# Kernel optimization log

Measured on AMD Instinct MI355X. Metric: run time of the kernel, lower is better.

## Reference

```python
import jax, jax.numpy as jnp
import numpy as np

N_NODES = 40000
N_EDGES = 640000
NFEAT = 128
NHID = 64  # gc1: NFEAT -> 2*NHID, gc2: 2*NHID -> NHID


def setup_inputs() -> dict:
    key = jax.random.key(0)
    ks = jax.random.split(key, 8)
    x = jax.random.normal(ks[0], (N_NODES, NFEAT), dtype=jnp.float32)
    edge_src = jax.random.randint(ks[1], (N_EDGES,), 0, N_NODES, dtype=jnp.int32)
    edge_dst = jax.random.randint(ks[2], (N_EDGES,), 0, N_NODES, dtype=jnp.int32)
    # normalized adjacency weights (e.g. D^-1/2 A D^-1/2 values), positive
    edge_weight = jax.random.uniform(ks[3], (N_EDGES,), dtype=jnp.float32)
    # Glorot-style init as in Kipf GraphConvolution (uniform +- 1/sqrt(fan_out))
    W1 = jax.random.uniform(ks[4], (NFEAT, 2 * NHID), dtype=jnp.float32,
                            minval=-1.0 / np.sqrt(2 * NHID), maxval=1.0 / np.sqrt(2 * NHID))
    b1 = jnp.zeros((2 * NHID,), dtype=jnp.float32)
    W2 = jax.random.uniform(ks[5], (2 * NHID, NHID), dtype=jnp.float32,
                            minval=-1.0 / np.sqrt(NHID), maxval=1.0 / np.sqrt(NHID))
    b2 = jnp.zeros((NHID,), dtype=jnp.float32)
    return {"x": x, "edge_src": edge_src, "edge_dst": edge_dst,
            "edge_weight": edge_weight, "W1": W1, "b1": b1, "W2": W2, "b2": b2}


def _gcn_layer(h, edge_src, edge_dst, edge_weight, W, b, n_nodes):
    # support = h @ W  (dense GEMM), then out = spmm(adj, support) + b
    support = h @ W                                   # [N, Dout]
    msgs = edge_weight[:, None] * support[edge_src]   # [E, Dout] gather
    agg = jax.ops.segment_sum(msgs, edge_dst, num_segments=n_nodes)  # scatter-add
    return agg + b


def reference(x, edge_src, edge_dst, edge_weight, W1, b1, W2, b2):
    n = x.shape[0]
    # gc1 -> relu -> dropout(eval: identity) -> gc2
    h = jax.nn.relu(_gcn_layer(x, edge_src, edge_dst, edge_weight, W1, b1, n))
    out = _gcn_layer(h, edge_src, edge_dst, edge_weight, W2, b2, n)
    return out
```

## Files before the change

kernel.cpp:

```cpp
#include <hip/hip_runtime.h>

#define N_NODES 40000
#define N_EDGES 640000
#define NFEAT   128
#define H1      128
#define H2      64

#define NBUCK   625
#define BCAP    2048
#define EPB     4096

#define OFF_SUP1   0UL
#define OFF_H      10240000UL
#define OFF_SUP2   20480000UL
#define OFF_BUCK   25600000UL
#define OFF_GCUR   35840000UL
#define OFF_W1T    35842560UL
#define OFF_W2T    35875328UL

typedef unsigned int uint;
typedef unsigned short ushort;
typedef __attribute__((ext_vector_type(8))) short bf16x8;
typedef __attribute__((ext_vector_type(4))) float f32x4;
typedef __attribute__((ext_vector_type(2))) float f32x2;

__device__ __forceinline__ float bl(uint u) { union { uint i; float f; } c; c.i = u << 16; return c.f; }
__device__ __forceinline__ float bh(uint u) { union { uint i; float f; } c; c.i = u & 0xFFFF0000u; return c.f; }
__device__ __forceinline__ ushort f2b(float f) {
    union { float f; uint i; } c; c.f = f;
    uint u = c.i + 0x7FFFu + ((c.i >> 16) & 1u);
    return (ushort)(u >> 16);
}

__global__ void init_k(uint* __restrict__ gcur,
                       const float* __restrict__ W1, const float* __restrict__ W2,
                       ushort* __restrict__ W1T, ushort* __restrict__ W2T) {
    const int i = blockIdx.x * 256 + threadIdx.x;
    if (i < NBUCK + 1) gcur[i] = 0;
    if (i < 128 * 128) {
        const int c = i >> 7, k = i & 127;
        W1T[i] = f2b(W1[k * 128 + c]);
    }
    if (i < 64 * 128) {
        const int c = i >> 7, k = i & 127;
        W2T[i] = f2b(W2[k * 64 + c]);
    }
}

__global__ __launch_bounds__(1024) void bin_k(const int* __restrict__ edst,
                                              const int* __restrict__ esrc,
                                              const float* __restrict__ ew,
                                              uint* __restrict__ gcur,
                                              uint2* __restrict__ buckets) {
    __shared__ uint2 stage[EPB];
    __shared__ uint cntL[NBUCK + 1];
    __shared__ uint offL[NBUCK + 1];
    __shared__ uint gbase[NBUCK + 1];
    __shared__ int wsum[16];
    const int t = threadIdx.x;
    const int lane = t & 63, wv = t >> 6;

    if (t < NBUCK + 1) cntL[t] = 0;
    __syncthreads();

    uint d_[4], rec_[4], rk_[4]; int b_[4];
#pragma unroll
    for (int k = 0; k < 4; ++k) {
        const int i = blockIdx.x * EPB + k * 1024 + t;
        uint d = 40000, rec = 0;
        if (i < N_EDGES) {
            d = (uint)edst[i];
            rec = ((uint)esrc[i] << 16) | (uint)f2b(ew[i]);
        }
        d_[k] = d; rec_[k] = rec; b_[k] = d >> 6;
        rk_[k] = atomicAdd(&cntL[b_[k]], 1u);
    }
    __syncthreads();

    {
        const int v = (t < NBUCK + 1) ? (int)cntL[t] : 0;
        int incl = v;
#pragma unroll
        for (int d = 1; d < 64; d <<= 1) {
            int o = __shfl_up(incl, d);
            if (lane >= d) incl += o;
        }
        if (lane == 63) wsum[wv] = incl;
        __syncthreads();
        if (t < 16) {
            int s = wsum[t];
#pragma unroll
            for (int d = 1; d < 16; d <<= 1) {
                int o = __shfl_up(s, d);
                if (t >= d) s += o;
            }
            wsum[t] = s;
        }
        __syncthreads();
        if (t < NBUCK + 1) {
            offL[t] = (uint)((wv ? wsum[wv - 1] : 0) + incl - v);
            gbase[t] = atomicAdd(&gcur[t], (uint)v);
        }
    }
    __syncthreads();

#pragma unroll
    for (int k = 0; k < 4; ++k) {
        uint2 s; s.x = d_[k]; s.y = rec_[k];
        stage[offL[b_[k]] + rk_[k]] = s;
    }
    __syncthreads();

#pragma unroll
    for (int k = 0; k < 4; ++k) {
        const int p = k * 1024 + t;
        const uint2 s = stage[p];
        const uint b = s.x >> 6;
        if (b < NBUCK) {
            const uint pos = gbase[b] + ((uint)p - offL[b]);
            if (pos < BCAP) buckets[(size_t)b * BCAP + pos] = s;
        }
    }
}

__global__ __launch_bounds__(256) void gemm1_k(const float* __restrict__ x,
                                               const ushort* __restrict__ WT,
                                               ushort* __restrict__ out) {
    const int lane = threadIdx.x & 63;
    const int m0 = blockIdx.x * 64 + (threadIdx.x >> 6) * 16;
    const int r = lane & 15, kg = lane >> 4;

    bf16x8 a[4];
    const float* xp = x + (size_t)(m0 + r) * 128 + kg * 8;
#pragma unroll
    for (int kt = 0; kt < 4; ++kt) {
        float xf[8];
        *(float4*)(xf)     = *(const float4*)(xp + kt * 32);
        *(float4*)(xf + 4) = *(const float4*)(xp + kt * 32 + 4);
        bf16x8 v;
#pragma unroll
        for (int i = 0; i < 8; ++i) v[i] = (short)f2b(xf[i]);
        a[kt] = v;
    }

#pragma unroll
    for (int nt = 0; nt < 8; ++nt) {
        const ushort* wp = WT + (size_t)(nt * 16 + r) * 128 + kg * 8;
        f32x4 acc = {0.f, 0.f, 0.f, 0.f};
#pragma unroll
        for (int kt = 0; kt < 4; ++kt) {
            const bf16x8 bfr = *(const bf16x8*)(wp + kt * 32);
            acc = __builtin_amdgcn_mfma_f32_16x16x32_bf16(a[kt], bfr, acc, 0, 0, 0);
        }
#pragma unroll
        for (int q = 0; q < 4; ++q)
            out[(size_t)(m0 + kg * 4 + q) * 128 + nt * 16 + r] = f2b(acc[q]);
    }
}

__global__ __launch_bounds__(256) void gemm2_k(const ushort* __restrict__ h,
                                               const ushort* __restrict__ WT,
                                               ushort* __restrict__ out) {
    const int lane = threadIdx.x & 63;
    const int m0 = blockIdx.x * 64 + (threadIdx.x >> 6) * 16;
    const int r = lane & 15, kg = lane >> 4;

    bf16x8 a[4];
    const ushort* hp = h + (size_t)(m0 + r) * 128 + kg * 8;
#pragma unroll
    for (int kt = 0; kt < 4; ++kt) a[kt] = *(const bf16x8*)(hp + kt * 32);

#pragma unroll
    for (int nt = 0; nt < 4; ++nt) {
        const ushort* wp = WT + (size_t)(nt * 16 + r) * 128 + kg * 8;
        f32x4 acc = {0.f, 0.f, 0.f, 0.f};
#pragma unroll
        for (int kt = 0; kt < 4; ++kt) {
            const bf16x8 bfr = *(const bf16x8*)(wp + kt * 32);
            acc = __builtin_amdgcn_mfma_f32_16x16x32_bf16(a[kt], bfr, acc, 0, 0, 0);
        }
#pragma unroll
        for (int q = 0; q < 4; ++q)
            out[(size_t)(m0 + kg * 4 + q) * 64 + nt * 16 + r] = f2b(acc[q]);
    }
}

__global__ __launch_bounds__(1024) void spmm1_k(const ushort* __restrict__ sup,
                                                const uint* __restrict__ gcur,
                                                const uint2* __restrict__ buckets,
                                                const float* __restrict__ b1,
                                                ushort* __restrict__ h) {
    __shared__ uint srt[BCAP];
    __shared__ uint cntL[64];
    __shared__ uint offL[64];
    const int t = threadIdx.x;
    const int bkt = blockIdx.x;
    if (t < 64) cntL[t] = 0;
    __syncthreads();

    const int cnt = min((int)gcur[bkt], BCAP);
    const uint2* bp = buckets + (size_t)bkt * BCAP;

    int n0 = -1, n1 = -1; uint rec0 = 0, rec1 = 0, rk0 = 0, rk1 = 0;
    if (t < cnt)        { const uint2 r = bp[t];        n0 = r.x & 63; rec0 = r.y; rk0 = atomicAdd(&cntL[n0], 1u); }
    if (t + 1024 < cnt) { const uint2 r = bp[t + 1024]; n1 = r.x & 63; rec1 = r.y; rk1 = atomicAdd(&cntL[n1], 1u); }
    __syncthreads();

    if (t < 64) {
        const int v = (int)cntL[t];
        int incl = v;
#pragma unroll
        for (int d = 1; d < 64; d <<= 1) {
            int o = __shfl_up(incl, d);
            if (t >= d) incl += o;
        }
        offL[t] = (uint)(incl - v);
    }
    __syncthreads();

    if (n0 >= 0) srt[offL[n0] + rk0] = rec0;
    if (n1 >= 0) srt[offL[n1] + rk1] = rec1;
    __syncthreads();

    const int lane = t & 63, wv = t >> 6;
    const uint* sup32 = (const uint*)sup;
    uint* h32 = (uint*)h;
    const float2 bb = ((const float2*)b1)[lane];
#pragma unroll
    for (int j = 0; j < 4; ++j) {
        const int n = wv * 4 + j;
        const int e0 = (int)offL[n], c = (int)cntL[n];
        float a0 = 0.f, a1 = 0.f, a2 = 0.f, a3 = 0.f;
        int e = 0;
        for (; e + 8 <= c; e += 8) {
            uint r[8], v[8];
#pragma unroll
            for (int k = 0; k < 8; ++k) r[k] = srt[e0 + e + k];
#pragma unroll
            for (int k = 0; k < 8; ++k) v[k] = sup32[((size_t)(r[k] >> 16) << 6) + lane];
#pragma unroll
            for (int k = 0; k < 8; k += 2) {
                const float w0 = bl(r[k]), w1 = bl(r[k + 1]);
                a0 = fmaf(w0, bl(v[k]), a0);     a1 = fmaf(w0, bh(v[k]), a1);
                a2 = fmaf(w1, bl(v[k + 1]), a2); a3 = fmaf(w1, bh(v[k + 1]), a3);
            }
        }
        for (; e + 4 <= c; e += 4) {
            uint r[4], v[4];
#pragma unroll
            for (int k = 0; k < 4; ++k) r[k] = srt[e0 + e + k];
#pragma unroll
            for (int k = 0; k < 4; ++k) v[k] = sup32[((size_t)(r[k] >> 16) << 6) + lane];
#pragma unroll
            for (int k = 0; k < 4; k += 2) {
                const float w0 = bl(r[k]), w1 = bl(r[k + 1]);
                a0 = fmaf(w0, bl(v[k]), a0);     a1 = fmaf(w0, bh(v[k]), a1);
                a2 = fmaf(w1, bl(v[k + 1]), a2); a3 = fmaf(w1, bh(v[k + 1]), a3);
            }
        }
        for (; e < c; ++e) {
            const uint r0 = srt[e0 + e];
            const uint v0 = sup32[((size_t)(r0 >> 16) << 6) + lane];
            a0 = fmaf(bl(r0), bl(v0), a0); a1 = fmaf(bl(r0), bh(v0), a1);
        }
        const float f0 = fmaxf((a0 + a2) + bb.x, 0.f);
        const float f1 = fmaxf((a1 + a3) + bb.y, 0.f);
        h32[(size_t)(bkt * 64 + n) * 64 + lane] = (uint)f2b(f0) | ((uint)f2b(f1) << 16);
    }
}

__global__ __launch_bounds__(1024) void spmm2_k(const ushort* __restrict__ sup,
                                                const uint* __restrict__ gcur,
                                                const uint2* __restrict__ buckets,
                                                const float* __restrict__ b2,
                                                float* __restrict__ out) {
    __shared__ uint srt[BCAP];
    __shared__ uint cntL[64];
    __shared__ uint offL[64];
    const int t = threadIdx.x;
    const int bkt = blockIdx.x;
    if (t < 64) cntL[t] = 0;
    __syncthreads();

    const int cnt = min((int)gcur[bkt], BCAP);
    const uint2* bp = buckets + (size_t)bkt * BCAP;

    int n0 = -1, n1 = -1; uint rec0 = 0, rec1 = 0, rk0 = 0, rk1 = 0;
    if (t < cnt)        { const uint2 r = bp[t];        n0 = r.x & 63; rec0 = r.y; rk0 = atomicAdd(&cntL[n0], 1u); }
    if (t + 1024 < cnt) { const uint2 r = bp[t + 1024]; n1 = r.x & 63; rec1 = r.y; rk1 = atomicAdd(&cntL[n1], 1u); }
    __syncthreads();

    if (t < 64) {
        const int v = (int)cntL[t];
        int incl = v;
#pragma unroll
        for (int d = 1; d < 64; d <<= 1) {
            int o = __shfl_up(incl, d);
            if (t >= d) incl += o;
        }
        offL[t] = (uint)(incl - v);
    }
    __syncthreads();

    if (n0 >= 0) srt[offL[n0] + rk0] = rec0;
    if (n1 >= 0) srt[offL[n1] + rk1] = rec1;
    __syncthreads();

    const int lane = t & 63, wv = t >> 6;
    const int hh = lane >> 5, l32 = lane & 31;
    const uint* sup32 = (const uint*)sup;
    const float2 bb = ((const float2*)b2)[l32];
#pragma unroll
    for (int j = 0; j < 4; ++j) {
        const int n = wv * 4 + j;
        const int e0 = (int)offL[n], c = (int)cntL[n];
        float d0 = 0.f, d1 = 0.f, d2 = 0.f, d3 = 0.f;
        int e = 0;
        for (; e + 8 <= c; e += 8) {
            const uint r0 = srt[e0 + e + hh],     r1 = srt[e0 + e + 2 + hh];
            const uint r2 = srt[e0 + e + 4 + hh], r3 = srt[e0 + e + 6 + hh];
            const uint v0 = sup32[((size_t)(r0 >> 16) << 5) + l32];
            const uint v1 = sup32[((size_t)(r1 >> 16) << 5) + l32];
            const uint v2 = sup32[((size_t)(r2 >> 16) << 5) + l32];
            const uint v3 = sup32[((size_t)(r3 >> 16) << 5) + l32];
            d0 = fmaf(bl(r0), bl(v0), d0); d1 = fmaf(bl(r0), bh(v0), d1);
            d2 = fmaf(bl(r1), bl(v1), d2); d3 = fmaf(bl(r1), bh(v1), d3);
            d0 = fmaf(bl(r2), bl(v2), d0); d1 = fmaf(bl(r2), bh(v2), d1);
            d2 = fmaf(bl(r3), bl(v3), d2); d3 = fmaf(bl(r3), bh(v3), d3);
        }
        for (; e + 2 <= c; e += 2) {
            const uint r0 = srt[e0 + e + hh];
            const uint v0 = sup32[((size_t)(r0 >> 16) << 5) + l32];
            d0 = fmaf(bl(r0), bl(v0), d0); d1 = fmaf(bl(r0), bh(v0), d1);
        }
        if (e < c && hh == 0) {
            const uint r0 = srt[e0 + e];
            const uint v0 = sup32[((size_t)(r0 >> 16) << 5) + l32];
            d0 = fmaf(bl(r0), bl(v0), d0); d1 = fmaf(bl(r0), bh(v0), d1);
        }
        float g0 = d0 + d2, g1 = d1 + d3;
        g0 += __shfl_xor(g0, 32); g1 += __shfl_xor(g1, 32);
        if (hh == 0) {
            f32x2 res = {g0 + bb.x, g1 + bb.y};
            __builtin_nontemporal_store(res, (f32x2*)out + (size_t)(bkt * 64 + n) * 32 + l32);
        }
    }
}

extern "C" void kernel_launch(void* const* d_in, const int* in_sizes, int n_in,
                              void* d_out, int out_size, void* d_ws, size_t ws_size,
                              hipStream_t stream) {
    const float* x    = (const float*)d_in[0];
    const int*   esrc = (const int*)d_in[1];
    const int*   edst = (const int*)d_in[2];
    const float* ew   = (const float*)d_in[3];
    const float* W1   = (const float*)d_in[4];
    const float* b1   = (const float*)d_in[5];
    const float* W2   = (const float*)d_in[6];
    const float* b2   = (const float*)d_in[7];
    float* out = (float*)d_out;

    char* ws = (char*)d_ws;
    ushort* sup1    = (ushort*)(ws + OFF_SUP1);
    ushort* h       = (ushort*)(ws + OFF_H);
    ushort* sup2    = (ushort*)(ws + OFF_SUP2);
    uint2*  buckets = (uint2*)(ws + OFF_BUCK);
    uint*   gcur    = (uint*)(ws + OFF_GCUR);
    ushort* W1T     = (ushort*)(ws + OFF_W1T);
    ushort* W2T     = (ushort*)(ws + OFF_W2T);

    init_k<<<64, 256, 0, stream>>>(gcur, W1, W2, W1T, W2T);
    bin_k<<<157, 1024, 0, stream>>>(edst, esrc, ew, gcur, buckets);

    gemm1_k<<<625, 256, 0, stream>>>(x, W1T, sup1);
    spmm1_k<<<NBUCK, 1024, 0, stream>>>(sup1, gcur, buckets, b1, h);

    gemm2_k<<<625, 256, 0, stream>>>(h, W2T, sup2);
    spmm2_k<<<NBUCK, 1024, 0, stream>>>(sup2, gcur, buckets, b2, out);
}
```

Measured before the change: 88.53 us.

## Fuse GEMM1 into binning launch and GEMM2 into first SpMM epilogue

```diff
diff --git a/kernel.cpp b/kernel.cpp
--- a/kernel.cpp
+++ b/kernel.cpp
@@ -9,14 +9,15 @@
 #define NBUCK   625
 #define BCAP    2048
 #define EPB     4096
+#define NBINB   157
+#define HPAD    68
 
 #define OFF_SUP1   0UL
-#define OFF_H      10240000UL
-#define OFF_SUP2   20480000UL
-#define OFF_BUCK   25600000UL
-#define OFF_GCUR   35840000UL
-#define OFF_W1T    35842560UL
-#define OFF_W2T    35875328UL
+#define OFF_SUP2   10240000UL
+#define OFF_BUCK   15360000UL
+#define OFF_GCUR   25600000UL
+#define OFF_W1T    25602560UL
+#define OFF_W2T    25635328UL
 
 typedef unsigned int uint;
 typedef unsigned short ushort;
@@ -47,11 +48,14 @@
     }
 }
 
-__global__ __launch_bounds__(1024) void bin_k(const int* __restrict__ edst,
-                                              const int* __restrict__ esrc,
-                                              const float* __restrict__ ew,
-                                              uint* __restrict__ gcur,
-                                              uint2* __restrict__ buckets) {
+__global__ __launch_bounds__(1024) void bingemm_k(const int* __restrict__ edst,
+                                                  const int* __restrict__ esrc,
+                                                  const float* __restrict__ ew,
+                                                  uint* __restrict__ gcur,
+                                                  uint2* __restrict__ buckets,
+                                                  const float* __restrict__ x,
+                                                  const ushort* __restrict__ W1T,
+                                                  ushort* __restrict__ sup1) {
     __shared__ uint2 stage[EPB];
     __shared__ uint cntL[NBUCK + 1];
     __shared__ uint offL[NBUCK + 1];
@@ -60,6 +64,40 @@
     const int t = threadIdx.x;
     const int lane = t & 63, wv = t >> 6;
 
+    if (blockIdx.x >= NBINB) {
+        const int gid = blockIdx.x - NBINB;
+        const int m0 = gid * 256 + wv * 16;
+        if (m0 >= N_NODES) return;
+        const int r = lane & 15, kg = lane >> 4;
+
+        bf16x8 a[4];
+        const float* xp = x + (size_t)(m0 + r) * 128 + kg * 8;
+#pragma unroll
+        for (int kt = 0; kt < 4; ++kt) {
+            float xf[8];
+            *(float4*)(xf)     = *(const float4*)(xp + kt * 32);
+            *(float4*)(xf + 4) = *(const float4*)(xp + kt * 32 + 4);
+            bf16x8 v;
+#pragma unroll
+            for (int i = 0; i < 8; ++i) v[i] = (short)f2b(xf[i]);
+            a[kt] = v;
+        }
+#pragma unroll
+        for (int nt = 0; nt < 8; ++nt) {
+            const ushort* wp = W1T + (size_t)(nt * 16 + r) * 128 + kg * 8;
+            f32x4 acc = {0.f, 0.f, 0.f, 0.f};
+#pragma unroll
+            for (int kt = 0; kt < 4; ++kt) {
+                const bf16x8 bfr = *(const bf16x8*)(wp + kt * 32);
+                acc = __builtin_amdgcn_mfma_f32_16x16x32_bf16(a[kt], bfr, acc, 0, 0, 0);
+            }
+#pragma unroll
+            for (int q = 0; q < 4; ++q)
+                sup1[(size_t)(m0 + kg * 4 + q) * 128 + nt * 16 + r] = f2b(acc[q]);
+        }
+        return;
+    }
+
     if (t < NBUCK + 1) cntL[t] = 0;
     __syncthreads();
 
@@ -123,74 +161,14 @@
     }
 }
 
-__global__ __launch_bounds__(256) void gemm1_k(const float* __restrict__ x,
-                                               const ushort* __restrict__ WT,
-                                               ushort* __restrict__ out) {
-    const int lane = threadIdx.x & 63;
-    const int m0 = blockIdx.x * 64 + (threadIdx.x >> 6) * 16;
-    const int r = lane & 15, kg = lane >> 4;
-
-    bf16x8 a[4];
-    const float* xp = x + (size_t)(m0 + r) * 128 + kg * 8;
-#pragma unroll
-    for (int kt = 0; kt < 4; ++kt) {
-        float xf[8];
-        *(float4*)(xf)     = *(const float4*)(xp + kt * 32);
-        *(float4*)(xf + 4) = *(const float4*)(xp + kt * 32 + 4);
-        bf16x8 v;
-#pragma unroll
-        for (int i = 0; i < 8; ++i) v[i] = (short)f2b(xf[i]);
-        a[kt] = v;
-    }
-
-#pragma unroll
-    for (int nt = 0; nt < 8; ++nt) {
-        const ushort* wp = WT + (size_t)(nt * 16 + r) * 128 + kg * 8;
-        f32x4 acc = {0.f, 0.f, 0.f, 0.f};
-#pragma unroll
-        for (int kt = 0; kt < 4; ++kt) {
-            const bf16x8 bfr = *(const bf16x8*)(wp + kt * 32);
-            acc = __builtin_amdgcn_mfma_f32_16x16x32_bf16(a[kt], bfr, acc, 0, 0, 0);
-        }
-#pragma unroll
-        for (int q = 0; q < 4; ++q)
-            out[(size_t)(m0 + kg * 4 + q) * 128 + nt * 16 + r] = f2b(acc[q]);
-    }
-}
-
-__global__ __launch_bounds__(256) void gemm2_k(const ushort* __restrict__ h,
-                                               const ushort* __restrict__ WT,
-                                               ushort* __restrict__ out) {
-    const int lane = threadIdx.x & 63;
-    const int m0 = blockIdx.x * 64 + (threadIdx.x >> 6) * 16;
-    const int r = lane & 15, kg = lane >> 4;
-
-    bf16x8 a[4];
-    const ushort* hp = h + (size_t)(m0 + r) * 128 + kg * 8;
-#pragma unroll
-    for (int kt = 0; kt < 4; ++kt) a[kt] = *(const bf16x8*)(hp + kt * 32);
-
-#pragma unroll
-    for (int nt = 0; nt < 4; ++nt) {
-        const ushort* wp = WT + (size_t)(nt * 16 + r) * 128 + kg * 8;
-        f32x4 acc = {0.f, 0.f, 0.f, 0.f};
-#pragma unroll
-        for (int kt = 0; kt < 4; ++kt) {
-            const bf16x8 bfr = *(const bf16x8*)(wp + kt * 32);
-            acc = __builtin_amdgcn_mfma_f32_16x16x32_bf16(a[kt], bfr, acc, 0, 0, 0);
-        }
-#pragma unroll
-        for (int q = 0; q < 4; ++q)
-            out[(size_t)(m0 + kg * 4 + q) * 64 + nt * 16 + r] = f2b(acc[q]);
-    }
-}
-
-__global__ __launch_bounds__(1024) void spmm1_k(const ushort* __restrict__ sup,
+__global__ __launch_bounds__(1024) void spmmg_k(const ushort* __restrict__ sup,
                                                 const uint* __restrict__ gcur,
                                                 const uint2* __restrict__ buckets,
                                                 const float* __restrict__ b1,
-                                                ushort* __restrict__ h) {
+                                                const ushort* __restrict__ W2T,
+                                                ushort* __restrict__ sup2) {
     __shared__ uint srt[BCAP];
+    __shared__ uint htile[64 * HPAD];
     __shared__ uint cntL[64];
     __shared__ uint offL[64];
     const int t = threadIdx.x;
@@ -224,7 +202,6 @@
 
     const int lane = t & 63, wv = t >> 6;
     const uint* sup32 = (const uint*)sup;
-    uint* h32 = (uint*)h;
     const float2 bb = ((const float2*)b1)[lane];
 #pragma unroll
     for (int j = 0; j < 4; ++j) {
@@ -265,7 +242,28 @@
         }
         const float f0 = fmaxf((a0 + a2) + bb.x, 0.f);
         const float f1 = fmaxf((a1 + a3) + bb.y, 0.f);
-        h32[(size_t)(bkt * 64 + n) * 64 + lane] = (uint)f2b(f0) | ((uint)f2b(f1) << 16);
+        htile[n * HPAD + lane] = (uint)f2b(f0) | ((uint)f2b(f1) << 16);
+    }
+    __syncthreads();
+
+    {
+        const int r = lane & 15, kg = lane >> 4;
+        const int rowtile = wv >> 2, ntile = wv & 3;
+        const uint* hrow = htile + (rowtile * 16 + r) * HPAD + kg * 4;
+        bf16x8 a[4];
+#pragma unroll
+        for (int kt = 0; kt < 4; ++kt) a[kt] = *(const bf16x8*)(hrow + kt * 16);
+
+        const ushort* wp = W2T + (size_t)(ntile * 16 + r) * 128 + kg * 8;
+        f32x4 acc = {0.f, 0.f, 0.f, 0.f};
+#pragma unroll
+        for (int kt = 0; kt < 4; ++kt) {
+            const bf16x8 bfr = *(const bf16x8*)(wp + kt * 32);
+            acc = __builtin_amdgcn_mfma_f32_16x16x32_bf16(a[kt], bfr, acc, 0, 0, 0);
+        }
+#pragma unroll
+        for (int q = 0; q < 4; ++q)
+            sup2[(size_t)(bkt * 64 + rowtile * 16 + kg * 4 + q) * 64 + ntile * 16 + r] = f2b(acc[q]);
     }
 }
 
@@ -362,7 +360,6 @@
 
     char* ws = (char*)d_ws;
     ushort* sup1    = (ushort*)(ws + OFF_SUP1);
-    ushort* h       = (ushort*)(ws + OFF_H);
     ushort* sup2    = (ushort*)(ws + OFF_SUP2);
     uint2*  buckets = (uint2*)(ws + OFF_BUCK);
     uint*   gcur    = (uint*)(ws + OFF_GCUR);
@@ -370,11 +367,7 @@
     ushort* W2T     = (ushort*)(ws + OFF_W2T);
 
     init_k<<<64, 256, 0, stream>>>(gcur, W1, W2, W1T, W2T);
-    bin_k<<<157, 1024, 0, stream>>>(edst, esrc, ew, gcur, buckets);
-
-    gemm1_k<<<625, 256, 0, stream>>>(x, W1T, sup1);
-    spmm1_k<<<NBUCK, 1024, 0, stream>>>(sup1, gcur, buckets, b1, h);
-
-    gemm2_k<<<625, 256, 0, stream>>>(h, W2T, sup2);
+    bingemm_k<<<NBINB + 157, 1024, 0, stream>>>(edst, esrc, ew, gcur, buckets, x, W1T, sup1);
+    spmmg_k<<<NBUCK, 1024, 0, stream>>>(sup1, gcur, buckets, b1, W2T, sup2);
     spmm2_k<<<NBUCK, 1024, 0, stream>>>(sup2, gcur, buckets, b2, out);
 }
```

After: 80.87 us. 8.7% less time.
